# Kernel optimization log

Hardware: AMD Instinct MI355X
Metric: run time of the kernel (lower is better)

The kernel has to match this reference:

```python
import jax, jax.numpy as jnp
import numpy as np

DIM = 512
NUM_HEADS = 16
WIN = (7, 7)
SIZE = WIN[0] * WIN[1]  # 49
B = 2048   # total windows
NW = 4     # windows per image (mask groups)


def _relative_position_index():
    coords_h = np.arange(WIN[0])
    coords_w = np.arange(WIN[1])
    coords = np.stack(np.meshgrid(coords_h, coords_w, indexing='ij'))  # [2,Wh,Ww]
    flat = coords.reshape(2, -1)                                       # [2,S]
    rel = flat[:, :, None] - flat[:, None, :]                          # [2,S,S]
    rel = rel.transpose(1, 2, 0)                                       # [S,S,2]
    rel[:, :, 0] += WIN[0] - 1
    rel[:, :, 1] += WIN[1] - 1
    rel[:, :, 0] *= 2 * WIN[1] - 1
    return rel.sum(-1).astype(np.int32)                                # [S,S]


def setup_inputs() -> dict:
    key = jax.random.key(0)
    ks = jax.random.split(key, 8)
    num_bias = (2 * WIN[0] - 1) * (2 * WIN[1] - 1)  # 169
    sd = 1.0 / np.sqrt(DIM)
    return {
        'x': jax.random.normal(ks[0], (B, SIZE, DIM), dtype=jnp.float32),
        'mask': jax.random.normal(ks[1], (NW, SIZE, SIZE), dtype=jnp.float32),
        'w_qkv': jax.random.normal(ks[2], (DIM, 3 * DIM), dtype=jnp.float32) * sd,
        'b_qkv': jnp.zeros((3 * DIM,), dtype=jnp.float32),
        'w_proj': jax.random.normal(ks[3], (DIM, DIM), dtype=jnp.float32) * sd,
        'b_proj': jnp.zeros((DIM,), dtype=jnp.float32),
        'bias_table': jax.random.normal(ks[4], (num_bias, NUM_HEADS), dtype=jnp.float32) * 0.02,
        'rel_idx': jnp.asarray(_relative_position_index()),
    }


def reference(x, mask, w_qkv, b_qkv, w_proj, b_proj, bias_table, rel_idx):
    b, s, c = x.shape
    h = NUM_HEADS
    hd = c // h
    scale = hd ** (-0.5)
    # qkv projection -> [3, B, H, S, hd]
    qkv = (x @ w_qkv + b_qkv).reshape(b, s, 3, h, hd).transpose(2, 0, 3, 1, 4)
    q, k, v = qkv[0] * scale, qkv[1], qkv[2]
    attn = jnp.einsum('bhqd,bhkd->bhqk', q, k)                 # [B,H,S,S]
    # gathered relative position bias -> [H,S,S]
    bias = bias_table[rel_idx.reshape(-1)].reshape(s, s, h).transpose(2, 0, 1)
    attn = attn + bias[None]
    nw = mask.shape[0]
    attn = attn.reshape(b // nw, nw, h, s, s) + mask[None, :, None]
    attn = jax.nn.softmax(attn.reshape(b, h, s, s), axis=-1)
    out = jnp.einsum('bhqk,bhkd->bhqd', attn, v)               # [B,H,S,hd]
    out = out.transpose(0, 2, 1, 3).reshape(b, s, c)
    return out @ w_proj + b_proj
```

## Files before the change

kernel.cpp:

```cpp
#include <hip/hip_runtime.h>
#include <hip/hip_bf16.h>
#include <stdint.h>

typedef float  floatx4 __attribute__((ext_vector_type(4)));
typedef short  short8  __attribute__((ext_vector_type(8)));
typedef unsigned short u16;

#define DIM 512
#define NH 16
#define HD 32
#define WS 49
#define NBW 2048
#define NWIN 4
#define M_TOTAL (NBW*WS)
#define N_QKV (3*DIM)

__device__ __forceinline__ u16 f2bf(float f) {
    uint32_t u = __float_as_uint(f);
    u += 0x7FFFu + ((u >> 16) & 1u);
    return (u16)(u >> 16);
}

__device__ __forceinline__ void load_lds16(const u16* g, u16* l) {
    __builtin_amdgcn_global_load_lds(
        (const __attribute__((address_space(1))) unsigned int*)g,
        (__attribute__((address_space(3))) unsigned int*)l, 16, 0, 0);
}

__global__ void cast_x_kernel(const float* __restrict__ in, u16* __restrict__ out, int n4) {
    int i = blockIdx.x * blockDim.x + threadIdx.x;
    if (i >= n4) return;
    const float4 v = ((const float4*)in)[i];
    ushort4 o;
    o.x = f2bf(v.x); o.y = f2bf(v.y); o.z = f2bf(v.z); o.w = f2bf(v.w);
    ((ushort4*)out)[i] = o;
}

__global__ void transpose_cast_kernel(const float* __restrict__ in, u16* __restrict__ out, int N) {
    __shared__ float t[32][33];
    const int bx = blockIdx.x * 32;
    const int by = blockIdx.y * 32;
    const int lx = threadIdx.x & 31;
    const int ly = threadIdx.x >> 5;
#pragma unroll
    for (int i = 0; i < 32; i += 8)
        t[ly + i][lx] = in[(long)(by + ly + i) * N + bx + lx];
    __syncthreads();
#pragma unroll
    for (int i = 0; i < 32; i += 8)
        out[(long)(bx + ly + i) * 512 + by + lx] = f2bf(t[lx][ly + i]);
}

__global__ void build_comb_kernel(const float* __restrict__ bias_table, const int* __restrict__ rel_idx,
                                  const float* __restrict__ mask, float* __restrict__ comb) {
    int idx = blockIdx.x * blockDim.x + threadIdx.x;
    if (idx >= NWIN * NH * 64 * 64) return;
    int c = idx & 3, jj = (idx >> 2) & 15, i = (idx >> 6) & 63, h = (idx >> 12) & 15, g = idx >> 16;
    int j = c * 16 + jj;
    float v = -1e30f;
    if (i < WS && j < WS)
        v = bias_table[rel_idx[i * WS + j] * NH + h] + mask[(g * WS + i) * WS + j];
    comb[idx] = v;
}

template<bool OUT_BF16>
__global__ __launch_bounds__(256, 2) void gemm_bt_kernel(
    const u16* __restrict__ A, const u16* __restrict__ Bt,
    const float* __restrict__ bias, void* __restrict__ out, int N, int K)
{
    __shared__ __align__(16) u16 sA[128 * 32];
    __shared__ __align__(16) u16 sB[128 * 32];
    const int tid  = threadIdx.x;
    const int lane = tid & 63;
    const int wave = tid >> 6;

    const int GXd = gridDim.x;
    const int nwg = GXd * gridDim.y;
    int fb = blockIdx.y * GXd + blockIdx.x;
    fb = (fb & 7) * (nwg >> 3) + (fb >> 3);
    const long m0 = (long)(fb / GXd) * 128;
    const long n0 = (long)(fb % GXd) * 128;

    const int rr = lane & 15;
    const int rq = lane >> 4;
    const int cs = (rq ^ ((lane >> 1) & 3)) * 8;
    const int wm = (wave >> 1) * 64;
    const int wn = (wave & 1) * 64;

    floatx4 acc[4][4];
    const floatx4 z4 = {0.f, 0.f, 0.f, 0.f};
#pragma unroll
    for (int mi = 0; mi < 4; ++mi)
#pragma unroll
        for (int ni = 0; ni < 4; ++ni) acc[mi][ni] = z4;

    const int row0 = tid >> 2;
    const int ssw  = ((tid & 3) ^ ((tid >> 3) & 3)) * 8;
    const u16* gA0 = A  + (m0 + row0) * K + ssw;
    const u16* gA1 = A  + (m0 + row0 + 64) * K + ssw;
    const u16* gB0 = Bt + (n0 + row0) * K + ssw;
    const u16* gB1 = Bt + (n0 + row0 + 64) * K + ssw;
    u16* lA0 = sA + tid * 8;
    u16* lA1 = sA + (tid + 256) * 8;
    u16* lB0 = sB + tid * 8;
    u16* lB1 = sB + (tid + 256) * 8;

    for (int k0 = 0; k0 < K; k0 += 32) {
        load_lds16(gA0 + k0, lA0);
        load_lds16(gA1 + k0, lA1);
        load_lds16(gB0 + k0, lB0);
        load_lds16(gB1 + k0, lB1);
        __syncthreads();
        short8 af[4], bfr[4];
#pragma unroll
        for (int mi = 0; mi < 4; ++mi)
            af[mi] = *(const short8*)(sA + (wm + mi * 16 + rr) * 32 + cs);
#pragma unroll
        for (int ni = 0; ni < 4; ++ni)
            bfr[ni] = *(const short8*)(sB + (wn + ni * 16 + rr) * 32 + cs);
#pragma unroll
        for (int mi = 0; mi < 4; ++mi)
#pragma unroll
            for (int ni = 0; ni < 4; ++ni)
                acc[mi][ni] = __builtin_amdgcn_mfma_f32_16x16x32_bf16(af[mi], bfr[ni], acc[mi][ni], 0, 0, 0);
        __syncthreads();
    }

#pragma unroll
    for (int mi = 0; mi < 4; ++mi) {
#pragma unroll
        for (int r = 0; r < 4; ++r) {
            const long m = m0 + wm + mi * 16 + rq * 4 + r;
#pragma unroll
            for (int ni = 0; ni < 4; ++ni) {
                const long n = n0 + wn + ni * 16 + rr;
                float v = acc[mi][ni][r] + bias[n];
                if (OUT_BF16) ((u16*)out)[m * N + n] = f2bf(v);
                else          ((float*)out)[m * N + n] = v;
            }
        }
    }
}

__global__ __launch_bounds__(256, 4) void attn_kernel(
    const u16* __restrict__ qkv, const float* __restrict__ comb,
    u16* __restrict__ attn_out)
{
    const int w   = threadIdx.x >> 6;
    const int l   = threadIdx.x & 63;
    const int job = blockIdx.x * 4 + w;
    const int b   = job >> 4;
    const int h   = job & 15;
    const int rr = l & 15;
    const int q4 = l >> 4;
    const int qk = q4 * 8;

    __shared__ __align__(16) u16 p_s[4][64 * 64];
    u16* ps = p_s[w];

    const u16* qg = qkv + (long)b * WS * N_QKV + h * HD;
    const u16* kg = qg + DIM;
    const u16* vg = qg + 2 * DIM;

    const short8 z8 = {0, 0, 0, 0, 0, 0, 0, 0};
    const floatx4 z4 = {0.f, 0.f, 0.f, 0.f};

    short8 bfr[4];
#pragma unroll
    for (int ni = 0; ni < 4; ++ni) {
        const int row = ni * 16 + rr;
        bfr[ni] = (row < WS) ? *(const short8*)(kg + (long)row * N_QKV + qk) : z8;
    }

    short8 vf[2][2];
#pragma unroll
    for (int kk = 0; kk < 2; ++kk)
#pragma unroll
        for (int ni = 0; ni < 2; ++ni) {
            short8 t = z8;
            const int d = 2 * rr + ni;
#pragma unroll
            for (int j = 0; j < 8; ++j) {
                const int s = kk * 32 + qk + j;
                if (s < WS) t[j] = (short)vg[(long)s * N_QKV + d];
            }
            vf[kk][ni] = t;
        }
    short8 vones;
#pragma unroll
    for (int j = 0; j < 8; ++j) vones[j] = (short)0x3F80;

    short8 af[4];
#pragma unroll
    for (int mi = 0; mi < 4; ++mi) {
        const int row = mi * 16 + rr;
        af[mi] = (row < WS) ? *(const short8*)(qg + (long)row * N_QKV + qk) : z8;
    }

    const float4* cb4 = (const float4*)comb + ((long)((b & (NWIN - 1)) * NH + h)) * 1024;
    const float scale = 0.17677669529663689f;

#pragma unroll
    for (int mi = 0; mi < 4; ++mi) {
        floatx4 scm[4];
#pragma unroll
        for (int ni = 0; ni < 4; ++ni)
            scm[ni] = __builtin_amdgcn_mfma_f32_16x16x32_bf16(af[mi], bfr[ni], z4, 0, 0, 0);
#pragma unroll
        for (int r = 0; r < 4; ++r) {
            const int il = mi * 16 + q4 * 4 + r;
            const float4 cb = cb4[il * 16 + rr];
            float e0 = __expf(scm[0][r] * scale + cb.x);
            float e1 = __expf(scm[1][r] * scale + cb.y);
            float e2 = __expf(scm[2][r] * scale + cb.z);
            float e3 = __expf(scm[3][r] * scale + cb.w);
#pragma unroll
            for (int c = 0; c < 4; ++c) {
                const int col = c * 16 + rr;
                const int blk = (col >> 3) ^ (il & 7);
                const float ev = (c == 0) ? e0 : (c == 1) ? e1 : (c == 2) ? e2 : e3;
                ps[il * 64 + blk * 8 + (col & 7)] = f2bf(ev);
            }
        }
    }
    asm volatile("s_waitcnt lgkmcnt(0)" ::: "memory");

    floatx4 oacc[4][3];
#pragma unroll
    for (int mi = 0; mi < 4; ++mi) { oacc[mi][0] = z4; oacc[mi][1] = z4; oacc[mi][2] = z4; }
#pragma unroll
    for (int kk = 0; kk < 2; ++kk) {
        short8 pf[4];
#pragma unroll
        for (int mi = 0; mi < 4; ++mi) {
            const int i2 = mi * 16 + rr;
            pf[mi] = *(const short8*)(ps + i2 * 64 + (((4 * kk + q4) ^ (i2 & 7)) * 8));
        }
#pragma unroll
        for (int mi = 0; mi < 4; ++mi) {
            oacc[mi][0] = __builtin_amdgcn_mfma_f32_16x16x32_bf16(pf[mi], vf[kk][0], oacc[mi][0], 0, 0, 0);
            oacc[mi][1] = __builtin_amdgcn_mfma_f32_16x16x32_bf16(pf[mi], vf[kk][1], oacc[mi][1], 0, 0, 0);
            oacc[mi][2] = __builtin_amdgcn_mfma_f32_16x16x32_bf16(pf[mi], vones,     oacc[mi][2], 0, 0, 0);
        }
    }

#pragma unroll
    for (int mi = 0; mi < 4; ++mi) {
#pragma unroll
        for (int r = 0; r < 4; ++r) {
            const int ig = mi * 16 + q4 * 4 + r;
            if (ig < WS) {
                const float inv = 1.0f / oacc[mi][2][r];
                const uint32_t lo = f2bf(oacc[mi][0][r] * inv);
                const uint32_t hi = f2bf(oacc[mi][1][r] * inv);
                uint32_t* op = (uint32_t*)(attn_out + ((long)(b * WS + ig)) * DIM + h * HD);
                op[rr] = lo | (hi << 16);
            }
        }
    }
}

extern "C" void kernel_launch(void* const* d_in, const int* in_sizes, int n_in,
                              void* d_out, int out_size, void* d_ws, size_t ws_size,
                              hipStream_t stream)
{
    const float* x          = (const float*)d_in[0];
    const float* mask       = (const float*)d_in[1];
    const float* w_qkv      = (const float*)d_in[2];
    const float* b_qkv      = (const float*)d_in[3];
    const float* w_proj     = (const float*)d_in[4];
    const float* b_proj     = (const float*)d_in[5];
    const float* bias_table = (const float*)d_in[6];
    const int*   rel_idx    = (const int*)d_in[7];
    float* out = (float*)d_out;

    char* ws = (char*)d_ws;
    u16* x_bf   = (u16*)ws;  ws += (size_t)M_TOTAL * DIM * 2;
    u16* wqkvT  = (u16*)ws;  ws += (size_t)N_QKV * DIM * 2;
    u16* wprojT = (u16*)ws;  ws += (size_t)DIM * DIM * 2;
    float* comb = (float*)ws; ws += (size_t)NWIN * NH * 64 * 64 * 4;
    u16* qkv    = (u16*)ws;  ws += (size_t)M_TOTAL * N_QKV * 2;
    u16* attn_o = x_bf;

    const int n4 = M_TOTAL * DIM / 4;
    cast_x_kernel<<<(n4 + 255) / 256, 256, 0, stream>>>(x, x_bf, n4);
    transpose_cast_kernel<<<dim3(N_QKV / 32, 16), 256, 0, stream>>>(w_qkv, wqkvT, N_QKV);
    transpose_cast_kernel<<<dim3(DIM / 32, 16), 256, 0, stream>>>(w_proj, wprojT, DIM);
    build_comb_kernel<<<(NWIN * NH * 64 * 64 + 255) / 256, 256, 0, stream>>>(bias_table, rel_idx, mask, comb);

    gemm_bt_kernel<true><<<dim3(N_QKV / 128, M_TOTAL / 128), 256, 0, stream>>>(
        x_bf, wqkvT, b_qkv, qkv, N_QKV, DIM);

    attn_kernel<<<NBW * NH / 4, 256, 0, stream>>>(qkv, comb, attn_o);

    gemm_bt_kernel<false><<<dim3(DIM / 128, M_TOTAL / 128), 256, 0, stream>>>(
        attn_o, wprojT, b_proj, out, DIM, DIM);
}
```

Before: 784.3 us.

## Triple-buffer LDS tiles in the bf16 GEMM with two-stage-ahead prefetch

The GEMM main loop previously loaded one K-slice into LDS, synchronised, computed, and synchronised again, so global-to-LDS latency was exposed on every iteration. It now keeps three LDS buffers and issues the direct-to-LDS loads two slices ahead. Explicit vmcnt waits and raw s_barrier calls replace __syncthreads, and s_setprio raises wave priority around the MFMA block. The cost is triple the LDS footprint per block, which could limit occupancy, plus reliance on hand-placed waitcnt and barrier ordering for correctness.

```diff
diff --git a/kernel.cpp b/kernel.cpp
--- a/kernel.cpp
+++ b/kernel.cpp
@@ -63,13 +63,21 @@
     comb[idx] = v;
 }
 
+#define STAGE32(BUF, K0)                                   \
+    do {                                                   \
+        load_lds16(gA0 + (K0), sA[BUF] + loff0);           \
+        load_lds16(gA1 + (K0), sA[BUF] + loff1);           \
+        load_lds16(gB0 + (K0), sB[BUF] + loff0);           \
+        load_lds16(gB1 + (K0), sB[BUF] + loff1);           \
+    } while (0)
+
 template<bool OUT_BF16>
 __global__ __launch_bounds__(256, 2) void gemm_bt_kernel(
     const u16* __restrict__ A, const u16* __restrict__ Bt,
     const float* __restrict__ bias, void* __restrict__ out, int N, int K)
 {
-    __shared__ __align__(16) u16 sA[128 * 32];
-    __shared__ __align__(16) u16 sB[128 * 32];
+    __shared__ __align__(16) u16 sA[3][128 * 32];
+    __shared__ __align__(16) u16 sB[3][128 * 32];
     const int tid  = threadIdx.x;
     const int lane = tid & 63;
     const int wave = tid >> 6;
@@ -100,30 +108,40 @@
     const u16* gA1 = A  + (m0 + row0 + 64) * K + ssw;
     const u16* gB0 = Bt + (n0 + row0) * K + ssw;
     const u16* gB1 = Bt + (n0 + row0 + 64) * K + ssw;
-    u16* lA0 = sA + tid * 8;
-    u16* lA1 = sA + (tid + 256) * 8;
-    u16* lB0 = sB + tid * 8;
-    u16* lB1 = sB + (tid + 256) * 8;
-
-    for (int k0 = 0; k0 < K; k0 += 32) {
-        load_lds16(gA0 + k0, lA0);
-        load_lds16(gA1 + k0, lA1);
-        load_lds16(gB0 + k0, lB0);
-        load_lds16(gB1 + k0, lB1);
-        __syncthreads();
+    const int loff0 = tid * 8;
+    const int loff1 = (tid + 256) * 8;
+
+    const int T = K >> 5;
+
+    STAGE32(0, 0);
+    STAGE32(1, 32);
+    asm volatile("s_waitcnt vmcnt(4)" ::: "memory");
+    __builtin_amdgcn_s_barrier();
+
+    int c = 0, n2 = 2;
+    for (int t = 0; t < T; ++t) {
+        const bool h2 = (t + 2 < T);
+        if (h2) STAGE32(n2, (t + 2) * 32);
         short8 af[4], bfr[4];
 #pragma unroll
         for (int mi = 0; mi < 4; ++mi)
-            af[mi] = *(const short8*)(sA + (wm + mi * 16 + rr) * 32 + cs);
+            af[mi] = *(const short8*)(sA[c] + (wm + mi * 16 + rr) * 32 + cs);
 #pragma unroll
         for (int ni = 0; ni < 4; ++ni)
-            bfr[ni] = *(const short8*)(sB + (wn + ni * 16 + rr) * 32 + cs);
+            bfr[ni] = *(const short8*)(sB[c] + (wn + ni * 16 + rr) * 32 + cs);
+        __builtin_amdgcn_s_barrier();
+        __builtin_amdgcn_s_setprio(1);
 #pragma unroll
         for (int mi = 0; mi < 4; ++mi)
 #pragma unroll
             for (int ni = 0; ni < 4; ++ni)
                 acc[mi][ni] = __builtin_amdgcn_mfma_f32_16x16x32_bf16(af[mi], bfr[ni], acc[mi][ni], 0, 0, 0);
-        __syncthreads();
+        __builtin_amdgcn_s_setprio(0);
+        if (h2) { asm volatile("s_waitcnt vmcnt(4)" ::: "memory"); }
+        else    { asm volatile("s_waitcnt vmcnt(0)" ::: "memory"); }
+        __builtin_amdgcn_s_barrier();
+        c  = (c  == 2) ? 0 : c  + 1;
+        n2 = (n2 == 2) ? 0 : n2 + 1;
     }
 
 #pragma unroll
```

After: 824.4 us. +5.1%, slower.
